# Kernel optimization log

Measured on AMD Instinct MI355X. Metric: run time of the kernel, lower is better.

## Reference

```python
import jax, jax.numpy as jnp
import numpy as np
from jax.scipy.linalg import expm

N, D, COND_DIM = 1152, 64, 1152
B, T = 16, 1024


def setup_inputs() -> dict:
    key = jax.random.key(0)
    k1, k2, k3, k4, k5 = jax.random.split(key, 5)
    x = jax.random.normal(k1, (B, T, N), dtype=jnp.float32)
    cond = jax.random.normal(k2, (B, COND_DIM), dtype=jnp.float32)
    # learned parameters
    P = jax.random.normal(k3, (N, D), dtype=jnp.float32)
    n_skew = D * (D - 1) // 2
    # nn.Linear default init: U(-1/sqrt(fan_in), 1/sqrt(fan_in))
    bound = 1.0 / np.sqrt(COND_DIM)
    W = jax.random.uniform(k4, (n_skew, COND_DIM), minval=-bound, maxval=bound, dtype=jnp.float32)
    b = jax.random.uniform(k5, (n_skew,), minval=-bound, maxval=bound, dtype=jnp.float32)
    return {"x": x, "cond": cond, "P": P, "W": W, "b": b}


def _rotation(cond, W, b):
    # SiLU -> Linear -> skew-symmetric A -> matrix exponential
    v = jax.nn.silu(cond) @ W.T + b  # (B, D*(D-1)//2)
    iu, ju = jnp.triu_indices(D, k=1)
    A = jnp.zeros((cond.shape[0], D, D), dtype=v.dtype)
    A = A.at[:, iu, ju].set(v).at[:, ju, iu].set(-v)
    return expm(A)  # batched over leading dim, (B, D, D)


def reference(x, cond, P, W, b):
    U, _ = jnp.linalg.qr(P)          # (N, D) orthonormal basis of subspace
    R = _rotation(cond, W, b)        # (B, D, D)
    z = jnp.einsum('btn,nd->btd', x, U)          # project into subspace
    z_rot = jnp.einsum('btd,bde->bte', z, R)     # rotate within subspace
    x_rot = x + jnp.einsum('btd,nd->btn', z_rot - z, U)  # (z_rot - z) @ U.T
    return x_rot
```

## Files before the change

kernel.cpp:

```cpp
#include <hip/hip_runtime.h>
#include <math.h>

#define NN 1152
#define DD 64
#define NSK 2016
#define NB 16
#define NROWS (NB*1024)
#define GPARTS 6
#define KPARTS 6
#define VNBLK 32
#define VBLKS (VNBLK*KPARTS)
#define TOFF (VBLKS + GPARTS)
#define TBLKS 18

typedef short bf16x8 __attribute__((ext_vector_type(8)));
typedef short bf16x4 __attribute__((ext_vector_type(4)));
typedef float f32x4  __attribute__((ext_vector_type(4)));

__device__ __forceinline__ short bfr(float f){
  unsigned u = __float_as_uint(f);
  u += 0x7fffu + ((u >> 16) & 1u);
  return (short)(u >> 16);
}
__device__ __forceinline__ float htof(short h){
  return __uint_as_float(((unsigned)(unsigned short)h) << 16);
}

__global__ __launch_bounds__(256) void k_pre(const float* __restrict__ cond, const float* __restrict__ W,
                                             float* __restrict__ vpart,
                                             const float* __restrict__ P, float* __restrict__ Gpart,
                                             short* __restrict__ Pbf, short* __restrict__ Ptbf){
  __shared__ float Ps[64*68];
  const int tid = threadIdx.x;
  if (blockIdx.x < VBLKS){
    const int nb = blockIdx.x / KPARTS;
    const int kp = blockIdx.x % KPARTS;
    const int lane = tid & 63, wid = tid >> 6;
    const int m = lane & 15, quad = lane >> 4;
    const int n0 = nb*64 + wid*16;
    if (n0 >= NSK) return;
    f32x4 acc = {0.f,0.f,0.f,0.f};
    const float* crow = &cond[m*NN + kp*192 + quad*8];
    const float* wrow = &W[(n0 + m)*NN + kp*192 + quad*8];
    #pragma unroll
    for (int c = 0; c < 6; ++c){
      const float4 ca = *(const float4*)(crow + c*32);
      const float4 cb = *(const float4*)(crow + c*32 + 4);
      const float4 wa = *(const float4*)(wrow + c*32);
      const float4 wb = *(const float4*)(wrow + c*32 + 4);
      bf16x8 a, b;
      const float cv[8] = {ca.x,ca.y,ca.z,ca.w,cb.x,cb.y,cb.z,cb.w};
      const float wv[8] = {wa.x,wa.y,wa.z,wa.w,wb.x,wb.y,wb.z,wb.w};
      #pragma unroll
      for (int j = 0; j < 8; ++j){
        const float xv = cv[j];
        a[j] = bfr(xv / (1.f + __expf(-xv)));
        b[j] = bfr(wv[j]);
      }
      acc = __builtin_amdgcn_mfma_f32_16x16x32_bf16(a, b, acc, 0, 0, 0);
    }
    #pragma unroll
    for (int r = 0; r < 4; ++r)
      vpart[(kp*16 + quad*4 + r)*NSK + n0 + m] = acc[r];
  } else if (blockIdx.x < TOFF){
    const int p = blockIdx.x - VBLKS;
    const int lr = tid >> 4, lc = (tid & 15) * 4;
    const int ti = tid >> 4, tj = tid & 15;
    float acc[4][4];
    #pragma unroll
    for (int i=0;i<4;++i){
      #pragma unroll
      for (int j=0;j<4;++j) acc[i][j]=0.f;
    }
    for (int ch = 0; ch < 3; ++ch){
      const int nn0 = p*192 + ch*64;
      __syncthreads();
      #pragma unroll
      for (int ii = 0; ii < 4; ++ii){
        const float4 pv = *(const float4*)&P[(nn0 + lr + 16*ii)*DD + lc];
        *(float4*)&Ps[(lr + 16*ii)*68 + lc] = pv;
      }
      __syncthreads();
      for (int r = 0; r < 64; ++r){
        const float4 a = *(const float4*)&Ps[r*68 + ti*4];
        const float4 b = *(const float4*)&Ps[r*68 + tj*4];
        const float av[4] = {a.x,a.y,a.z,a.w};
        const float bv[4] = {b.x,b.y,b.z,b.w};
        #pragma unroll
        for (int i=0;i<4;++i){
          #pragma unroll
          for (int j=0;j<4;++j) acc[i][j] = fmaf(av[i], bv[j], acc[i][j]);
        }
      }
    }
    float* g = &Gpart[p*DD*DD];
    #pragma unroll
    for (int i=0;i<4;++i){
      float4 ov = make_float4(acc[i][0], acc[i][1], acc[i][2], acc[i][3]);
      *(float4*)&g[(ti*4+i)*DD + tj*4] = ov;
    }
  } else {
    const int t = blockIdx.x - TOFF;
    const int n0 = t*64;
    for (int idx = tid; idx < 4096; idx += 256)
      Ps[(idx>>6)*68 + (idx&63)] = P[(n0 + (idx>>6))*DD + (idx&63)];
    __syncthreads();
    for (int idx = tid; idx < 4096; idx += 256){
      const int r = idx>>6, c = idx&63;
      Pbf[(n0+r)*DD + c] = bfr(Ps[r*68 + c]);
    }
    for (int idx = tid; idx < 4096; idx += 256){
      const int d = idx>>6, rr = idx&63;
      Ptbf[d*NN + n0 + rr] = bfr(Ps[rr*68 + d]);
    }
  }
}

__device__ __forceinline__ void mmul68(const float* __restrict__ A, const float* __restrict__ B,
                                       float* __restrict__ C, int tid){
  __syncthreads();
  const int w = tid >> 6, lane = tid & 63;
  const int r0 = (w & 3) * 16 + (lane >> 3) * 2;
  const int c0 = (w >> 2) * 32 + (lane & 7) * 4;
  float acc[2][4];
  #pragma unroll
  for (int i=0;i<2;++i){
    #pragma unroll
    for (int j=0;j<4;++j) acc[i][j]=0.f;
  }
  float4 b0 = *(const float4*)&B[0*68 + c0];
  float4 b1 = *(const float4*)&B[1*68 + c0];
  float4 b2 = *(const float4*)&B[2*68 + c0];
  float4 b3 = *(const float4*)&B[3*68 + c0];
  float4 a0 = *(const float4*)&A[(r0    )*68];
  float4 a1 = *(const float4*)&A[(r0 + 1)*68];
  for (int kq = 0; kq < 16; ++kq){
    float4 nb0, nb1, nb2, nb3, na0, na1;
    if (kq < 15){
      const int k4 = (kq+1)*4;
      nb0 = *(const float4*)&B[(k4+0)*68 + c0];
      nb1 = *(const float4*)&B[(k4+1)*68 + c0];
      nb2 = *(const float4*)&B[(k4+2)*68 + c0];
      nb3 = *(const float4*)&B[(k4+3)*68 + c0];
      na0 = *(const float4*)&A[(r0    )*68 + k4];
      na1 = *(const float4*)&A[(r0 + 1)*68 + k4];
    }
    const float av0[4] = {a0.x,a0.y,a0.z,a0.w};
    const float av1[4] = {a1.x,a1.y,a1.z,a1.w};
    const float4 bb[4] = {b0,b1,b2,b3};
    #pragma unroll
    for (int kk=0;kk<4;++kk){
      acc[0][0] = fmaf(av0[kk], bb[kk].x, acc[0][0]);
      acc[0][1] = fmaf(av0[kk], bb[kk].y, acc[0][1]);
      acc[0][2] = fmaf(av0[kk], bb[kk].z, acc[0][2]);
      acc[0][3] = fmaf(av0[kk], bb[kk].w, acc[0][3]);
      acc[1][0] = fmaf(av1[kk], bb[kk].x, acc[1][0]);
      acc[1][1] = fmaf(av1[kk], bb[kk].y, acc[1][1]);
      acc[1][2] = fmaf(av1[kk], bb[kk].z, acc[1][2]);
      acc[1][3] = fmaf(av1[kk], bb[kk].w, acc[1][3]);
    }
    b0 = nb0; b1 = nb1; b2 = nb2; b3 = nb3; a0 = na0; a1 = na1;
  }
  *(float4*)&C[(r0    )*68 + c0] = make_float4(acc[0][0],acc[0][1],acc[0][2],acc[0][3]);
  *(float4*)&C[(r0 + 1)*68 + c0] = make_float4(acc[1][0],acc[1][1],acc[1][2],acc[1][3]);
  __syncthreads();
}

__global__ __launch_bounds__(512,1) void k_fused(const float* __restrict__ Gpart, const float* __restrict__ P,
                                                 const float* __restrict__ vpart, const float* __restrict__ bias,
                                                 float* __restrict__ Mg, float* __restrict__ Rg,
                                                 const float* __restrict__ x, const short* __restrict__ Ptbf,
                                                 short* __restrict__ ybf){
  __shared__ float Bs[64*68], B2[64*68], B3[64*68], Tb[64*68], Xb[64*68];
  __shared__ float red[512];
  __shared__ float scl_s;
  __shared__ int   ssh_s;
  const int tid = threadIdx.x;
  if (blockIdx.x > NB){
    const int lane = tid & 63, wid = tid >> 6;
    const int row0 = (blockIdx.x - NB - 1) * 64;
    const int m    = lane & 15, quad = lane >> 4;
    const int r0 = (wid & 3) * 16;
    const int c0 = (wid >> 2) * 32;
    f32x4 acc0 = {0.f,0.f,0.f,0.f}, acc1 = {0.f,0.f,0.f,0.f};
    const float* xrow = &x[(row0 + r0 + m)*NN + quad*8];
    const short* ut0  = &Ptbf[(c0      + m)*NN + quad*8];
    const short* ut1  = &Ptbf[(c0 + 16 + m)*NN + quad*8];
    float4 xa = *(const float4*)(xrow);
    float4 xb = *(const float4*)(xrow + 4);
    bf16x8 b0 = *(const bf16x8*)(ut0);
    bf16x8 b1 = *(const bf16x8*)(ut1);
    for (int kc = 0; kc < NN; kc += 32){
      float4 nxa, nxb; bf16x8 nb0, nb1;
      if (kc + 32 < NN){
        nxa = *(const float4*)(xrow + kc + 32);
        nxb = *(const float4*)(xrow + kc + 36);
        nb0 = *(const bf16x8*)(ut0 + kc + 32);
        nb1 = *(const bf16x8*)(ut1 + kc + 32);
      }
      bf16x8 a;
      a[0]=bfr(xa.x); a[1]=bfr(xa.y); a[2]=bfr(xa.z); a[3]=bfr(xa.w);
      a[4]=bfr(xb.x); a[5]=bfr(xb.y); a[6]=bfr(xb.z); a[7]=bfr(xb.w);
      acc0 = __builtin_amdgcn_mfma_f32_16x16x32_bf16(a, b0, acc0, 0, 0, 0);
      acc1 = __builtin_amdgcn_mfma_f32_16x16x32_bf16(a, b1, acc1, 0, 0, 0);
      xa = nxa; xb = nxb; b0 = nb0; b1 = nb1;
    }
    #pragma unroll
    for (int q = 0; q < 4; ++q){
      ybf[(row0 + r0 + quad*4 + q)*DD + c0      + m] = bfr(acc0[q]);
      ybf[(row0 + r0 + quad*4 + q)*DD + c0 + 16 + m] = bfr(acc1[q]);
    }
    return;
  }
  if (blockIdx.x == NB){
    if (tid < 64){
      const int j = tid;
      float Gc[DD], Wc[DD], Rc[DD];
      #pragma unroll
      for (int i = 0; i < DD; ++i){
        float g = 0.f;
        #pragma unroll
        for (int p = 0; p < GPARTS; ++p) g += Gpart[p*4096 + i*DD + j];
        Gc[i] = g;
        Wc[i] = P[i*DD + j];
      }
      #pragma unroll
      for (int k = 0; k < DD; ++k){
        const float gkk = __shfl(Gc[k], k);
        const float wkk = __shfl(Wc[k], k);
        const float beta = (wkk >= 0.f) ? -sqrtf(gkk) : sqrtf(gkk);
        const float wkj = Wc[k];
        const float dj  = Gc[k] - beta*wkj;
        const float cj  = dj / (beta*(beta - wkk));
        float rkj = wkj + dj/beta;
        if (j == k) rkj = beta;
        if (j <  k) rkj = 0.f;
        Rc[k] = rkj;
        #pragma unroll
        for (int i = k+1; i < DD; ++i){
          const float wik = __shfl(Wc[i], k);
          const float rki = __shfl(rkj, i);
          Wc[i] = fmaf(-cj,  wik, Wc[i]);
          Gc[i] = fmaf(-rki, rkj, Gc[i]);
        }
      }
      #pragma unroll
      for (int i = 0; i < DD; ++i) Rg[i*DD + j] = Rc[i];
    }
    return;
  }
  const int b = blockIdx.x;
  for (int idx = tid; idx < 64*64; idx += 512)
    Xb[(idx>>6)*68 + (idx&63)] = 0.f;
  __syncthreads();
  for (int idx = tid; idx < NSK; idx += 512){
    int i = (int)((127.0f - sqrtf(16129.0f - 8.0f*(float)idx)) * 0.5f);
    while (i*(127 - i)/2 > idx) --i;
    while ((i+1)*(127 - (i+1))/2 <= idx) ++i;
    const int jj = idx - i*(127 - i)/2 + i + 1;
    float val = bias[idx];
    #pragma unroll
    for (int p = 0; p < KPARTS; ++p) val += vpart[(p*16 + b)*NSK + idx];
    Xb[i*68 + jj] = val;
    Xb[jj*68 + i] = -val;
  }
  __syncthreads();
  {
    const int c = tid & 63, g = tid >> 6;
    float s = 0.f;
    for (int r = g*8; r < g*8 + 8; ++r) s += fabsf(Xb[r*68 + c]);
    red[g*64 + c] = s;
    __syncthreads();
    if (tid < 64){
      float cs = 0.f;
      #pragma unroll
      for (int g2 = 0; g2 < 8; ++g2) cs += red[g2*64 + tid];
      #pragma unroll
      for (int off = 32; off > 0; off >>= 1) cs = fmaxf(cs, __shfl_xor(cs, off));
      if (tid == 0){
        int s2 = 0; float scale = 1.f;
        float nrm = cs;
        while (nrm > 1.0f && s2 < 40){ nrm *= 0.5f; scale *= 0.5f; ++s2; }
        ssh_s = s2; scl_s = scale;
      }
    }
    __syncthreads();
  }
  const float scale = scl_s;
  const int   sq    = ssh_s;
  for (int idx = tid; idx < 64*64; idx += 512){
    const int i = idx>>6, jj = idx&63;
    Bs[i*68 + jj] = Xb[i*68 + jj] * scale;
  }
  mmul68(Bs, Bs, B2, tid);
  mmul68(B2, Bs, B3, tid);
  for (int idx = tid; idx < 64*64; idx += 512){
    const int i = idx>>6, jj = idx&63;
    const int o = i*68 + jj;
    Tb[o] = (i==jj ? (1.f/720.f) : 0.f) + Bs[o]*(1.f/5040.f) + B2[o]*(1.f/40320.f) + B3[o]*(1.f/362880.f);
  }
  mmul68(B3, Tb, Xb, tid);
  for (int idx = tid; idx < 64*64; idx += 512){
    const int i = idx>>6, jj = idx&63;
    const int o = i*68 + jj;
    Xb[o] += (i==jj ? (1.f/6.f) : 0.f) + Bs[o]*(1.f/24.f) + B2[o]*(1.f/120.f);
  }
  mmul68(B3, Xb, Tb, tid);
  for (int idx = tid; idx < 64*64; idx += 512){
    const int i = idx>>6, jj = idx&63;
    const int o = i*68 + jj;
    Tb[o] += (i==jj ? 1.f : 0.f) + Bs[o] + B2[o]*0.5f;
  }
  float* cur = Tb;
  float* oth = Xb;
  for (int r = 0; r < sq; ++r){
    mmul68(cur, cur, oth, tid);
    float* t = cur; cur = oth; oth = t;
  }
  for (int idx = tid; idx < 64*64; idx += 512){
    const int i = idx>>6, jj = idx&63;
    Mg[b*4096 + idx] = cur[i*68 + jj] - (i==jj ? 1.f : 0.f);
  }
}

__global__ __launch_bounds__(256) void k_kmat(const float* __restrict__ Rg, const float* __restrict__ Mg,
                                              const short* __restrict__ Pbf, short* __restrict__ Qtbf){
  __shared__ float Ri[64*68], Ms[64*68], Ts[64*68];
  __shared__ short Kbf[64*72];
  __shared__ float rd[64];
  const int b = blockIdx.x, tid = threadIdx.x;
  const int lane = tid & 63, wid = tid >> 6;
  const int m = lane & 15, quad = lane >> 4;
  float* Rf = Ts;
  for (int idx = tid; idx < 4096; idx += 256){
    Rf[idx] = Rg[idx];
    Ms[(idx>>6)*68 + (idx&63)] = Mg[b*4096 + idx];
  }
  __syncthreads();
  if (tid < 64) rd[tid] = 1.f / Rf[tid*DD + tid];
  __syncthreads();
  if (tid < 64){
    float u[DD];
    #pragma unroll
    for (int j = 0; j < DD; ++j){
      float s0 = (tid == j) ? 1.f : 0.f, s1 = 0.f;
      #pragma unroll
      for (int l = 0; l + 1 < j; l += 2){
        s0 = fmaf(-u[l],   Rf[l*DD + j],     s0);
        s1 = fmaf(-u[l+1], Rf[(l+1)*DD + j], s1);
      }
      if (j & 1) s0 = fmaf(-u[j-1], Rf[(j-1)*DD + j], s0);
      u[j] = (s0 + s1) * rd[j];
    }
    #pragma unroll
    for (int c = 0; c < DD; ++c) Ri[tid*68 + c] = u[c];
  }
  __syncthreads();
  const int ti = tid >> 4, tj = tid & 15;
  {
    float acc[4][4];
    #pragma unroll
    for (int i=0;i<4;++i){
      #pragma unroll
      for (int j=0;j<4;++j) acc[i][j]=0.f;
    }
    for (int kq = 0; kq < 16; ++kq){
      float4 a[4], bm[4];
      #pragma unroll
      for (int i=0;i<4;++i) a[i] = *(const float4*)&Ri[(ti*4+i)*68 + kq*4];
      #pragma unroll
      for (int kk=0;kk<4;++kk) bm[kk] = *(const float4*)&Ms[(kq*4+kk)*68 + tj*4];
      #pragma unroll
      for (int i=0;i<4;++i){
        const float av[4] = {a[i].x,a[i].y,a[i].z,a[i].w};
        #pragma unroll
        for (int kk=0;kk<4;++kk){
          acc[i][0] = fmaf(av[kk], bm[kk].x, acc[i][0]);
          acc[i][1] = fmaf(av[kk], bm[kk].y, acc[i][1]);
          acc[i][2] = fmaf(av[kk], bm[kk].z, acc[i][2]);
          acc[i][3] = fmaf(av[kk], bm[kk].w, acc[i][3]);
        }
      }
    }
    __syncthreads();
    #pragma unroll
    for (int i=0;i<4;++i)
      *(float4*)&Ts[(ti*4+i)*68 + tj*4] = make_float4(acc[i][0],acc[i][1],acc[i][2],acc[i][3]);
    __syncthreads();
  }
  {
    float acc[4][4];
    #pragma unroll
    for (int i=0;i<4;++i){
      #pragma unroll
      for (int j=0;j<4;++j) acc[i][j]=0.f;
    }
    for (int kq = 0; kq < 16; ++kq){
      float4 a[4], bt[4];
      #pragma unroll
      for (int i=0;i<4;++i) a[i] = *(const float4*)&Ts[(ti*4+i)*68 + kq*4];
      #pragma unroll
      for (int j=0;j<4;++j) bt[j] = *(const float4*)&Ri[(tj*4+j)*68 + kq*4];
      #pragma unroll
      for (int i=0;i<4;++i){
        #pragma unroll
        for (int j=0;j<4;++j){
          acc[i][j] = fmaf(a[i].x, bt[j].x, acc[i][j]);
          acc[i][j] = fmaf(a[i].y, bt[j].y, acc[i][j]);
          acc[i][j] = fmaf(a[i].z, bt[j].z, acc[i][j]);
          acc[i][j] = fmaf(a[i].w, bt[j].w, acc[i][j]);
        }
      }
    }
    #pragma unroll
    for (int i=0;i<4;++i)
      #pragma unroll
      for (int j=0;j<4;++j)
        Kbf[(ti*4+i)*72 + tj*4+j] = bfr(acc[i][j]);
  }
  __syncthreads();
  for (int ch = 0; ch < 18; ++ch){
    const int n0 = ch*64;
    const bf16x8 a0 = *(const bf16x8*)&Pbf[(n0 + wid*16 + m)*DD +      quad*8];
    const bf16x8 a1 = *(const bf16x8*)&Pbf[(n0 + wid*16 + m)*DD + 32 + quad*8];
    #pragma unroll
    for (int ct = 0; ct < 4; ++ct){
      const bf16x8 b0 = *(const bf16x8*)&Kbf[(ct*16 + m)*72 +      quad*8];
      const bf16x8 b1 = *(const bf16x8*)&Kbf[(ct*16 + m)*72 + 32 + quad*8];
      f32x4 acc = {0.f,0.f,0.f,0.f};
      acc = __builtin_amdgcn_mfma_f32_16x16x32_bf16(a0, b0, acc, 0, 0, 0);
      acc = __builtin_amdgcn_mfma_f32_16x16x32_bf16(a1, b1, acc, 0, 0, 0);
      #pragma unroll
      for (int q = 0; q < 4; ++q)
        Ms[(wid*16 + quad*4 + q)*68 + ct*16 + m] = acc[q];
    }
    __syncthreads();
    {
      const int r = tid >> 2, c16 = (tid & 3) * 16;
      bf16x8 p0, p1;
      #pragma unroll
      for (int j = 0; j < 8; ++j){
        p0[j] = bfr(Ms[r*68 + c16 + j]);
        p1[j] = bfr(Ms[r*68 + c16 + 8 + j]);
      }
      *(bf16x8*)&Qtbf[(b*NN + n0 + r)*DD + c16]     = p0;
      *(bf16x8*)&Qtbf[(b*NN + n0 + r)*DD + c16 + 8] = p1;
    }
    __syncthreads();
  }
}

__global__ __launch_bounds__(256) void k_out2(const float* __restrict__ x, const short* __restrict__ Qtbf,
                                              const short* __restrict__ ybf, float* __restrict__ out){
  const int tid  = threadIdx.x;
  const int lane = tid & 63, wid = tid >> 6;
  const int row0 = blockIdx.x * 16;
  const int bb   = row0 >> 10;
  const int m    = lane & 15, quad = lane >> 4;
  const int q4   = quad * 4;
  const short* Qb = &Qtbf[bb*NN*DD];
  bf16x8 ya0 = *(const bf16x8*)&ybf[(row0 + m)*DD +      quad*8];
  bf16x8 ya1 = *(const bf16x8*)&ybf[(row0 + m)*DD + 32 + quad*8];
  bf16x8 qb0 = *(const bf16x8*)&Qb[(wid*16 + m)*DD +      quad*8];
  bf16x8 qb1 = *(const bf16x8*)&Qb[(wid*16 + m)*DD + 32 + quad*8];
  float xq0 = x[(row0 + q4 + 0)*NN + wid*16 + m];
  float xq1 = x[(row0 + q4 + 1)*NN + wid*16 + m];
  float xq2 = x[(row0 + q4 + 2)*NN + wid*16 + m];
  float xq3 = x[(row0 + q4 + 3)*NN + wid*16 + m];
  for (int it = 0; it < 18; ++it){
    const int n0 = (wid + 4*it) * 16;
    f32x4 acc = {0.f,0.f,0.f,0.f};
    acc = __builtin_amdgcn_mfma_f32_16x16x32_bf16(ya0, qb0, acc, 0, 0, 0);
    acc = __builtin_amdgcn_mfma_f32_16x16x32_bf16(ya1, qb1, acc, 0, 0, 0);
    const float o0 = xq0 + acc[0];
    const float o1 = xq1 + acc[1];
    const float o2 = xq2 + acc[2];
    const float o3 = xq3 + acc[3];
    if (it < 17){
      const int n1 = n0 + 64;
      qb0 = *(const bf16x8*)&Qb[(n1 + m)*DD +      quad*8];
      qb1 = *(const bf16x8*)&Qb[(n1 + m)*DD + 32 + quad*8];
      xq0 = x[(row0 + q4 + 0)*NN + n1 + m];
      xq1 = x[(row0 + q4 + 1)*NN + n1 + m];
      xq2 = x[(row0 + q4 + 2)*NN + n1 + m];
      xq3 = x[(row0 + q4 + 3)*NN + n1 + m];
    }
    out[(row0 + q4 + 0)*NN + n0 + m] = o0;
    out[(row0 + q4 + 1)*NN + n0 + m] = o1;
    out[(row0 + q4 + 2)*NN + n0 + m] = o2;
    out[(row0 + q4 + 3)*NN + n0 + m] = o3;
  }
}

extern "C" void kernel_launch(void* const* d_in, const int* in_sizes, int n_in,
                              void* d_out, int out_size, void* d_ws, size_t ws_size,
                              hipStream_t stream) {
  const float* x    = (const float*)d_in[0];
  const float* cond = (const float*)d_in[1];
  const float* P    = (const float*)d_in[2];
  const float* W    = (const float*)d_in[3];
  const float* bias = (const float*)d_in[4];
  float* out = (float*)d_out;
  float* ws  = (float*)d_ws;

  float* Gpart = ws;
  float* vpart = ws + 24576;
  float* Mg    = ws + 218112;
  float* Rg    = ws + 283648;
  short* Pbf   = (short*)(ws + 287744);
  short* Ptbf  = (short*)(ws + 324608);
  short* ybf   = (short*)(ws + 361472);
  short* Qtbf  = (short*)(ws + 885760);

  hipLaunchKernelGGL(k_pre,  dim3(VBLKS + GPARTS + TBLKS), dim3(256), 0, stream,
                     cond, W, vpart, P, Gpart, Pbf, Ptbf);
  hipLaunchKernelGGL(k_fused, dim3(NB + 1 + NROWS/64), dim3(512), 0, stream,
                     Gpart, P, vpart, bias, Mg, Rg, x, Ptbf, ybf);
  hipLaunchKernelGGL(k_kmat, dim3(NB), dim3(256), 0, stream, Rg, Mg, Pbf, Qtbf);
  hipLaunchKernelGGL(k_out2, dim3(NROWS/16), dim3(256), 0, stream, x, Qtbf, ybf, out);
}
```

Baseline: 250.4 us.

## Split Q^T build into parallel kernel and stage output via LDS for float4 I/O

The per-batch K matrix is now written to global memory in fp32, and a new kernel spreads the 1152x64 Qt product across 16x18 blocks instead of 16 serial blocks. The output kernel stages each 16x64 MFMA tile in double-buffered shared memory so x loads and out stores become row-contiguous float4 accesses. This adds a kernel launch, a barrier per iteration, and drops the software prefetch of Q and x. Kg reuses the vpart workspace region, which is assumed dead by that point.

```diff
diff --git a/kernel.cpp b/kernel.cpp
--- a/kernel.cpp
+++ b/kernel.cpp
@@ -324,13 +324,10 @@
 }
 
 __global__ __launch_bounds__(256) void k_kmat(const float* __restrict__ Rg, const float* __restrict__ Mg,
-                                              const short* __restrict__ Pbf, short* __restrict__ Qtbf){
+                                              float* __restrict__ Kg){
   __shared__ float Ri[64*68], Ms[64*68], Ts[64*68];
-  __shared__ short Kbf[64*72];
   __shared__ float rd[64];
   const int b = blockIdx.x, tid = threadIdx.x;
-  const int lane = tid & 63, wid = tid >> 6;
-  const int m = lane & 15, quad = lane >> 4;
   float* Rf = Ts;
   for (int idx = tid; idx < 4096; idx += 256){
     Rf[idx] = Rg[idx];
@@ -414,81 +411,79 @@
     }
     #pragma unroll
     for (int i=0;i<4;++i)
-      #pragma unroll
-      for (int j=0;j<4;++j)
-        Kbf[(ti*4+i)*72 + tj*4+j] = bfr(acc[i][j]);
-  }
-  __syncthreads();
-  for (int ch = 0; ch < 18; ++ch){
-    const int n0 = ch*64;
-    const bf16x8 a0 = *(const bf16x8*)&Pbf[(n0 + wid*16 + m)*DD +      quad*8];
-    const bf16x8 a1 = *(const bf16x8*)&Pbf[(n0 + wid*16 + m)*DD + 32 + quad*8];
-    #pragma unroll
-    for (int ct = 0; ct < 4; ++ct){
-      const bf16x8 b0 = *(const bf16x8*)&Kbf[(ct*16 + m)*72 +      quad*8];
-      const bf16x8 b1 = *(const bf16x8*)&Kbf[(ct*16 + m)*72 + 32 + quad*8];
-      f32x4 acc = {0.f,0.f,0.f,0.f};
-      acc = __builtin_amdgcn_mfma_f32_16x16x32_bf16(a0, b0, acc, 0, 0, 0);
-      acc = __builtin_amdgcn_mfma_f32_16x16x32_bf16(a1, b1, acc, 0, 0, 0);
-      #pragma unroll
-      for (int q = 0; q < 4; ++q)
-        Ms[(wid*16 + quad*4 + q)*68 + ct*16 + m] = acc[q];
-    }
-    __syncthreads();
-    {
-      const int r = tid >> 2, c16 = (tid & 3) * 16;
-      bf16x8 p0, p1;
-      #pragma unroll
-      for (int j = 0; j < 8; ++j){
-        p0[j] = bfr(Ms[r*68 + c16 + j]);
-        p1[j] = bfr(Ms[r*68 + c16 + 8 + j]);
-      }
-      *(bf16x8*)&Qtbf[(b*NN + n0 + r)*DD + c16]     = p0;
-      *(bf16x8*)&Qtbf[(b*NN + n0 + r)*DD + c16 + 8] = p1;
-    }
-    __syncthreads();
-  }
-}
-
-__global__ __launch_bounds__(256) void k_out2(const float* __restrict__ x, const short* __restrict__ Qtbf,
+      *(float4*)&Kg[b*4096 + (ti*4+i)*DD + tj*4] = make_float4(acc[i][0],acc[i][1],acc[i][2],acc[i][3]);
+  }
+}
+
+__global__ __launch_bounds__(256) void k_qt(const float* __restrict__ Kg, const short* __restrict__ Pbf,
+                                            short* __restrict__ Qtbf){
+  __shared__ short Kbf[64*72];
+  __shared__ float Qs[64*68];
+  const int b  = blockIdx.x / 18;
+  const int ch = blockIdx.x % 18;
+  const int tid = threadIdx.x;
+  const int lane = tid & 63, wid = tid >> 6;
+  const int m = lane & 15, quad = lane >> 4;
+  for (int idx = tid; idx < 4096; idx += 256)
+    Kbf[(idx>>6)*72 + (idx&63)] = bfr(Kg[b*4096 + idx]);
+  __syncthreads();
+  const int n0 = ch*64;
+  const bf16x8 a0 = *(const bf16x8*)&Pbf[(n0 + wid*16 + m)*DD +      quad*8];
+  const bf16x8 a1 = *(const bf16x8*)&Pbf[(n0 + wid*16 + m)*DD + 32 + quad*8];
+  #pragma unroll
+  for (int ct = 0; ct < 4; ++ct){
+    const bf16x8 b0 = *(const bf16x8*)&Kbf[(ct*16 + m)*72 +      quad*8];
+    const bf16x8 b1 = *(const bf16x8*)&Kbf[(ct*16 + m)*72 + 32 + quad*8];
+    f32x4 acc = {0.f,0.f,0.f,0.f};
+    acc = __builtin_amdgcn_mfma_f32_16x16x32_bf16(a0, b0, acc, 0, 0, 0);
+    acc = __builtin_amdgcn_mfma_f32_16x16x32_bf16(a1, b1, acc, 0, 0, 0);
+    #pragma unroll
+    for (int q = 0; q < 4; ++q)
+      Qs[(wid*16 + quad*4 + q)*68 + ct*16 + m] = acc[q];
+  }
+  __syncthreads();
+  {
+    const int r = tid >> 2, c16 = (tid & 3) * 16;
+    bf16x8 p0, p1;
+    #pragma unroll
+    for (int j = 0; j < 8; ++j){
+      p0[j] = bfr(Qs[r*68 + c16 + j]);
+      p1[j] = bfr(Qs[r*68 + c16 + 8 + j]);
+    }
+    *(bf16x8*)&Qtbf[(b*NN + n0 + r)*DD + c16]     = p0;
+    *(bf16x8*)&Qtbf[(b*NN + n0 + r)*DD + c16 + 8] = p1;
+  }
+}
+
+__global__ __launch_bounds__(256) void k_out3(const float* __restrict__ x, const short* __restrict__ Qtbf,
                                               const short* __restrict__ ybf, float* __restrict__ out){
+  __shared__ float os[2][16*68];
   const int tid  = threadIdx.x;
   const int lane = tid & 63, wid = tid >> 6;
   const int row0 = blockIdx.x * 16;
   const int bb   = row0 >> 10;
   const int m    = lane & 15, quad = lane >> 4;
-  const int q4   = quad * 4;
+  const int er = tid >> 4;
+  const int ec = (tid & 15) * 4;
   const short* Qb = &Qtbf[bb*NN*DD];
   bf16x8 ya0 = *(const bf16x8*)&ybf[(row0 + m)*DD +      quad*8];
   bf16x8 ya1 = *(const bf16x8*)&ybf[(row0 + m)*DD + 32 + quad*8];
-  bf16x8 qb0 = *(const bf16x8*)&Qb[(wid*16 + m)*DD +      quad*8];
-  bf16x8 qb1 = *(const bf16x8*)&Qb[(wid*16 + m)*DD + 32 + quad*8];
-  float xq0 = x[(row0 + q4 + 0)*NN + wid*16 + m];
-  float xq1 = x[(row0 + q4 + 1)*NN + wid*16 + m];
-  float xq2 = x[(row0 + q4 + 2)*NN + wid*16 + m];
-  float xq3 = x[(row0 + q4 + 3)*NN + wid*16 + m];
   for (int it = 0; it < 18; ++it){
-    const int n0 = (wid + 4*it) * 16;
+    const int n0 = it*64 + wid*16;
+    const bf16x8 qb0 = *(const bf16x8*)&Qb[(n0 + m)*DD +      quad*8];
+    const bf16x8 qb1 = *(const bf16x8*)&Qb[(n0 + m)*DD + 32 + quad*8];
     f32x4 acc = {0.f,0.f,0.f,0.f};
     acc = __builtin_amdgcn_mfma_f32_16x16x32_bf16(ya0, qb0, acc, 0, 0, 0);
     acc = __builtin_amdgcn_mfma_f32_16x16x32_bf16(ya1, qb1, acc, 0, 0, 0);
-    const float o0 = xq0 + acc[0];
-    const float o1 = xq1 + acc[1];
-    const float o2 = xq2 + acc[2];
-    const float o3 = xq3 + acc[3];
-    if (it < 17){
-      const int n1 = n0 + 64;
-      qb0 = *(const bf16x8*)&Qb[(n1 + m)*DD +      quad*8];
-      qb1 = *(const bf16x8*)&Qb[(n1 + m)*DD + 32 + quad*8];
-      xq0 = x[(row0 + q4 + 0)*NN + n1 + m];
-      xq1 = x[(row0 + q4 + 1)*NN + n1 + m];
-      xq2 = x[(row0 + q4 + 2)*NN + n1 + m];
-      xq3 = x[(row0 + q4 + 3)*NN + n1 + m];
-    }
-    out[(row0 + q4 + 0)*NN + n0 + m] = o0;
-    out[(row0 + q4 + 1)*NN + n0 + m] = o1;
-    out[(row0 + q4 + 2)*NN + n0 + m] = o2;
-    out[(row0 + q4 + 3)*NN + n0 + m] = o3;
+    float* ob = os[it & 1];
+    #pragma unroll
+    for (int q = 0; q < 4; ++q)
+      ob[(quad*4 + q)*68 + wid*16 + m] = acc[q];
+    __syncthreads();
+    const float4 xv = *(const float4*)&x[(row0 + er)*NN + it*64 + ec];
+    const float4 ov = *(const float4*)&ob[er*68 + ec];
+    *(float4*)&out[(row0 + er)*NN + it*64 + ec] =
+        make_float4(xv.x + ov.x, xv.y + ov.y, xv.z + ov.z, xv.w + ov.w);
   }
 }
 
@@ -505,6 +500,7 @@
 
   float* Gpart = ws;
   float* vpart = ws + 24576;
+  float* Kg    = ws + 24576;
   float* Mg    = ws + 218112;
   float* Rg    = ws + 283648;
   short* Pbf   = (short*)(ws + 287744);
@@ -516,6 +512,7 @@
                      cond, W, vpart, P, Gpart, Pbf, Ptbf);
   hipLaunchKernelGGL(k_fused, dim3(NB + 1 + NROWS/64), dim3(512), 0, stream,
                      Gpart, P, vpart, bias, Mg, Rg, x, Ptbf, ybf);
-  hipLaunchKernelGGL(k_kmat, dim3(NB), dim3(256), 0, stream, Rg, Mg, Pbf, Qtbf);
-  hipLaunchKernelGGL(k_out2, dim3(NROWS/16), dim3(256), 0, stream, x, Qtbf, ybf, out);
-}
+  hipLaunchKernelGGL(k_kmat, dim3(NB), dim3(256), 0, stream, Rg, Mg, Kg);
+  hipLaunchKernelGGL(k_qt,  dim3(NB*18), dim3(256), 0, stream, Kg, Pbf, Qtbf);
+  hipLaunchKernelGGL(k_out3, dim3(NROWS/16), dim3(256), 0, stream, x, Qtbf, ybf, out);
+}
```

New measurement: 239.6 us. 1.05x faster.
